# Optimization experiments

Measured on AMD Instinct MI355X. Metric: run time of the kernel, lower is better.

Reference implementation:

```python
import jax, jax.numpy as jnp
import numpy as np

N = 50000      # nodes
E = 800000     # edges
IN = 128       # in_channels
HID = 128      # hidden_channels
OUT = 2        # out_channels (edge classes)
HEADS = 8      # EGConv default num_heads
BASES = 4      # EGConv default num_bases
FH = HID // HEADS  # per-head feature dim = 16


def _egconv(x, Wb, Wc, bc, b, row, col, norm, n):
    """One EGConv layer (aggregators=['symnorm']), self-loops already in row/col/norm.
    Wb: [in, BASES*FH] basis projection (no bias).
    Wc: [in, HEADS*BASES], bc: combination weights linear.
    b : [HID] output bias.
    """
    bases = x @ Wb                                            # [n, BASES*FH]
    msg = bases[row] * norm[:, None]                          # gather + symnorm scale
    agg = jax.ops.segment_sum(msg, col, num_segments=n)       # scatter-add -> [n, BASES*FH]
    w = (x @ Wc + bc).reshape(n, HEADS, BASES)                # per-node combination weights
    out = jnp.einsum('nhb,nbf->nhf', w, agg.reshape(n, BASES, FH))
    return out.reshape(n, HEADS * FH) + b


def setup_inputs() -> dict:
    key = jax.random.key(0)
    ks = jax.random.split(key, 12)
    s = 0.05
    inp = {
        'x': jax.random.normal(ks[0], (N, IN), jnp.float32),
        'edge_index': jax.random.randint(ks[1], (2, E), 0, N, jnp.int64),
        # conv1
        'Wb1': jax.random.normal(ks[2], (IN, BASES * FH), jnp.float32) * s,
        'Wc1': jax.random.normal(ks[3], (IN, HEADS * BASES), jnp.float32) * s,
        'bc1': jnp.zeros((HEADS * BASES,), jnp.float32),
        'b1': jnp.zeros((HID,), jnp.float32),
        # conv2
        'Wb2': jax.random.normal(ks[4], (HID, BASES * FH), jnp.float32) * s,
        'Wc2': jax.random.normal(ks[5], (HID, HEADS * BASES), jnp.float32) * s,
        'bc2': jnp.zeros((HEADS * BASES,), jnp.float32),
        'b2': jnp.zeros((HID,), jnp.float32),
        # edge classifier
        'Wcls': jax.random.normal(ks[6], (2 * HID, OUT), jnp.float32) * s,
        'bcls': jnp.zeros((OUT,), jnp.float32),
    }
    return inp


def reference(x, edge_index, Wb1, Wc1, bc1, b1, Wb2, Wc2, bc2, b2, Wcls, bcls):
    n = x.shape[0]
    # add self loops (EGConv default add_self_loops=True) + gcn_norm symnorm weights
    sl = jnp.arange(n, dtype=edge_index.dtype)
    row = jnp.concatenate([edge_index[0], sl])
    col = jnp.concatenate([edge_index[1], sl])
    deg = jax.ops.segment_sum(jnp.ones(row.shape[0], x.dtype), col, num_segments=n)
    dis = jnp.where(deg > 0, deg, 1.0) ** -0.5
    dis = jnp.where(deg > 0, dis, 0.0)
    norm = dis[row] * dis[col]                                # symnorm edge weight

    h = jax.nn.relu(_egconv(x, Wb1, Wc1, bc1, b1, row, col, norm, n))
    h = _egconv(h, Wb2, Wc2, bc2, b2, row, col, norm, n)

    # edge classifier: gather endpoint embeddings of ORIGINAL edges, concat, linear
    e = jnp.concatenate([h[edge_index[0]], h[edge_index[1]]], axis=-1)  # [E, 2*HID]
    return e @ Wcls + bcls
```

## Files before the change

kernel.cpp:

```cpp
#include <hip/hip_runtime.h>
#include <hip/hip_fp16.h>

#define NN 50000
#define NNP 50048
#define EE 800000
#define CH 32
#define CHE (EE / CH)
#define NB_E2 1563
#define NWIN 4
#define WIN 12500
#define EPB 1024
#define NCHUNK 782

__global__ __launch_bounds__(256) void k_count(
    const int* __restrict__ ei, unsigned* __restrict__ pk, int* __restrict__ part)
{
    __shared__ int hist[WIN];
    int c = blockIdx.x >> 2;
    int w = blockIdx.x & 3;
    int tid = threadIdx.x;
    for (int i = tid; i < WIN; i += 256) hist[i] = 0;
    __syncthreads();
    int e0 = c * CHE;
    unsigned lo = w * WIN;
    const int* cols = ei + EE + e0;
    for (int i = tid; i < CHE / 4; i += 256) {
        int4 cc = *(const int4*)(cols + i * 4);
        unsigned d;
        d = (unsigned)cc.x - lo;
        if (d < WIN) {
            int r = atomicAdd(&hist[d], 1);
            pk[e0 + i * 4 + 0] = (unsigned)cc.x | ((unsigned)c << 16) | ((unsigned)r << 21);
        }
        d = (unsigned)cc.y - lo;
        if (d < WIN) {
            int r = atomicAdd(&hist[d], 1);
            pk[e0 + i * 4 + 1] = (unsigned)cc.y | ((unsigned)c << 16) | ((unsigned)r << 21);
        }
        d = (unsigned)cc.z - lo;
        if (d < WIN) {
            int r = atomicAdd(&hist[d], 1);
            pk[e0 + i * 4 + 2] = (unsigned)cc.z | ((unsigned)c << 16) | ((unsigned)r << 21);
        }
        d = (unsigned)cc.w - lo;
        if (d < WIN) {
            int r = atomicAdd(&hist[d], 1);
            pk[e0 + i * 4 + 3] = (unsigned)cc.w | ((unsigned)c << 16) | ((unsigned)r << 21);
        }
    }
    __syncthreads();
    int* pc = part + (size_t)c * NNP + lo;
    for (int i = tid; i < WIN; i += 256) pc[i] = hist[i];
}

__global__ void k_reduce(const int* __restrict__ part, int* __restrict__ cnt,
                         float* __restrict__ dis) {
    int i = blockIdx.x * 256 + threadIdx.x;
    if (i >= NN) return;
    int v = 0;
#pragma unroll
    for (int c = 0; c < CH; c++) v += part[(size_t)c * NNP + i];
    cnt[i] = v;
    dis[i] = rsqrtf((float)v + 1.0f);
}

__global__ void k_scan(const int* __restrict__ cnt, const int* __restrict__ part,
                       int2* __restrict__ sd, int* __restrict__ chunkstart, int n) {
    __shared__ int s[256];
    int tid = threadIdx.x, b = blockIdx.x;
    int i = b * 256 + tid;
    int v = (i < n) ? cnt[i] : 0;
    s[tid] = v;
    __syncthreads();
    for (int off = 1; off < 256; off <<= 1) {
        int t2 = (tid >= off) ? s[tid - off] : 0;
        __syncthreads();
        if (tid >= off) s[tid] += t2;
        __syncthreads();
    }
    int loc = s[tid] - v;
    int lim = b * 256;
    int pre = 0;
    for (int j = tid * 4; j < lim; j += 1024) {
        int4 c4 = *(const int4*)(cnt + j);
        pre += c4.x + c4.y + c4.z + c4.w;
    }
    __syncthreads();
    s[tid] = pre;
    __syncthreads();
    for (int off = 128; off; off >>= 1) {
        if (tid < off) s[tid] += s[tid + off];
        __syncthreads();
    }
    int boff = s[0];
    if (i < n) {
        int st = loc + boff;
        sd[i] = make_int2(st, v);
        int cs = st;
#pragma unroll
        for (int c = 0; c < CH; c++) {
            chunkstart[(size_t)c * NNP + i] = cs;
            cs += part[(size_t)c * NNP + i];
        }
    }
}

__global__ __launch_bounds__(256) void k_fill(
    const int* __restrict__ ei, const unsigned* __restrict__ pk,
    const int* __restrict__ chunkstart, int* __restrict__ csr)
{
    int w = blockIdx.x & (NWIN - 1);
    int chunk = blockIdx.x >> 2;
    int base = chunk * EPB + threadIdx.x * 4;
    unsigned lo = w * WIN;
    if (base + 3 < EE) {
        int4 rr = *(const int4*)(ei + base);
        uint4 pp = *(const uint4*)(pk + base);
        unsigned c0 = pp.x & 0xffffu, c1 = pp.y & 0xffffu;
        unsigned c2 = pp.z & 0xffffu, c3 = pp.w & 0xffffu;
        if (c0 - lo < WIN) csr[chunkstart[(size_t)((pp.x >> 16) & 31u) * NNP + c0] + (pp.x >> 21)] = rr.x;
        if (c1 - lo < WIN) csr[chunkstart[(size_t)((pp.y >> 16) & 31u) * NNP + c1] + (pp.y >> 21)] = rr.y;
        if (c2 - lo < WIN) csr[chunkstart[(size_t)((pp.z >> 16) & 31u) * NNP + c2] + (pp.z >> 21)] = rr.z;
        if (c3 - lo < WIN) csr[chunkstart[(size_t)((pp.w >> 16) & 31u) * NNP + c3] + (pp.w >> 21)] = rr.w;
    } else {
        for (int e = 0; e < 4; e++) {
            int t = base + e;
            if (t < EE) {
                unsigned pv = pk[t];
                unsigned cgl = pv & 0xffffu;
                if (cgl - lo < WIN)
                    csr[chunkstart[(size_t)((pv >> 16) & 31u) * NNP + cgl] + (pv >> 21)] = ei[t];
            }
        }
    }
}

__global__ __launch_bounds__(256) void k_gemm(
    const float* __restrict__ x, const float* __restrict__ Wb,
    const float* __restrict__ Wc, const float* __restrict__ bc,
    const float* __restrict__ dis,
    __half* __restrict__ bsh, float* __restrict__ wcomb, int n)
{
    int tid = threadIdx.x;
    int grp = blockIdx.y;
    int row = blockIdx.x * 256 + tid;
    bool valid = row < n;
    const float* xr = x + (size_t)(valid ? row : (n - 1)) * 128;

    const float* W = (grp < 2) ? (Wb + grp * 32) : Wc;
    const int ldw = (grp < 2) ? 64 : 32;

    float acc[32];
#pragma unroll
    for (int c = 0; c < 32; c++) acc[c] = 0.f;

    for (int s = 0; s < 4; s++) {
        float4 v[8];
#pragma unroll
        for (int j = 0; j < 8; j++)
            v[j] = *(const float4*)(xr + s * 32 + j * 4);
        const float* Ws = W + s * 32 * ldw;
#pragma unroll 8
        for (int k = 0; k < 32; k++) {
            float xs = ((const float*)v)[k];
            const float* wk = Ws + k * ldw;
#pragma unroll
            for (int c = 0; c < 32; c++) acc[c] = fmaf(xs, wk[c], acc[c]);
        }
    }

    if (!valid) return;
    if (grp < 2) {
        float d = dis[row];
        __half2 hh[16];
#pragma unroll
        for (int c = 0; c < 16; c++)
            hh[c] = __floats2half2_rn(acc[2 * c] * d, acc[2 * c + 1] * d);
        uint4* bo = (uint4*)(bsh + (size_t)row * 64 + grp * 32);
        const uint4* src = (const uint4*)hh;
#pragma unroll
        for (int c = 0; c < 4; c++) bo[c] = src[c];
    } else {
        float4* wo = (float4*)(wcomb + (size_t)row * 32);
#pragma unroll
        for (int c = 0; c < 8; c++)
            wo[c] = make_float4(acc[4*c] + bc[4*c], acc[4*c+1] + bc[4*c+1],
                                acc[4*c+2] + bc[4*c+2], acc[4*c+3] + bc[4*c+3]);
    }
}

template<int LAYER2>
__global__ __launch_bounds__(256) void k_agg(
    const int* __restrict__ csr, const int2* __restrict__ sd,
    const __half* __restrict__ bsh, const float* __restrict__ dis,
    const float* __restrict__ wcomb, const float* __restrict__ bias,
    float* __restrict__ h,
    const float* __restrict__ Wcls, const float* __restrict__ bcls,
    float* __restrict__ p, int n)
{
    int wid = (blockIdx.x * 256 + threadIdx.x) >> 6;
    int lane = threadIdx.x & 63;
    if (wid >= n) return;
    int2 s2 = sd[wid];
    int start = s2.x, deg = s2.y;
    int g = lane >> 4, q = lane & 15;

    const uint2* bsp = (const uint2*)bsh;
    float4 acc4 = make_float4(0.f, 0.f, 0.f, 0.f);
    if (g == 0) {
        uint2 v = bsp[(size_t)wid * 16 + q];
        float2 lo = __half22float2(*(const __half2*)&v.x);
        float2 hi = __half22float2(*(const __half2*)&v.y);
        acc4 = make_float4(lo.x, lo.y, hi.x, hi.y);
    }

    int j = 0;
    int ia = 0, ib = 0;
    if (8 <= deg) { ia = csr[start + g]; ib = csr[start + 4 + g]; }
    while (j + 8 <= deg) {
        int jn = j + 8;
        int na = 0, nb = 0;
        if (jn + 8 <= deg) { na = csr[start + jn + g]; nb = csr[start + jn + 4 + g]; }
        uint2 v0 = bsp[(size_t)ia * 16 + q];
        uint2 v1 = bsp[(size_t)ib * 16 + q];
        float2 l0 = __half22float2(*(const __half2*)&v0.x);
        float2 h0 = __half22float2(*(const __half2*)&v0.y);
        float2 l1 = __half22float2(*(const __half2*)&v1.x);
        float2 h1 = __half22float2(*(const __half2*)&v1.y);
        acc4.x += l0.x + l1.x;
        acc4.y += l0.y + l1.y;
        acc4.z += h0.x + h1.x;
        acc4.w += h0.y + h1.y;
        ia = na; ib = nb; j = jn;
    }
    int last = start + deg - 1;
    for (; j < deg; j += 4) {
        int idx = start + j + g;
        int r = csr[min(idx, last)];
        uint2 v = bsp[(size_t)r * 16 + q];
        float2 lo = __half22float2(*(const __half2*)&v.x);
        float2 hi = __half22float2(*(const __half2*)&v.y);
        float m = (j + g < deg) ? 1.f : 0.f;
        acc4.x = fmaf(lo.x, m, acc4.x);
        acc4.y = fmaf(lo.y, m, acc4.y);
        acc4.z = fmaf(hi.x, m, acc4.z);
        acc4.w = fmaf(hi.y, m, acc4.w);
    }

    acc4.x += __shfl_xor(acc4.x, 16, 64);
    acc4.y += __shfl_xor(acc4.y, 16, 64);
    acc4.z += __shfl_xor(acc4.z, 16, 64);
    acc4.w += __shfl_xor(acc4.w, 16, 64);
    acc4.x += __shfl_xor(acc4.x, 32, 64);
    acc4.y += __shfl_xor(acc4.y, 32, 64);
    acc4.z += __shfl_xor(acc4.z, 32, 64);
    acc4.w += __shfl_xor(acc4.w, 32, 64);

    float d = dis[wid];
    acc4.x *= d; acc4.y *= d; acc4.z *= d; acc4.w *= d;

    int src = lane >> 2;
    float t0 = __shfl(acc4.x, src, 64);
    float t1 = __shfl(acc4.y, src, 64);
    float t2 = __shfl(acc4.z, src, 64);
    float t3 = __shfl(acc4.w, src, 64);
    int c = lane & 3;
    float acc = (c == 0) ? t0 : (c == 1) ? t1 : (c == 2) ? t2 : t3;

    int fh = lane & 15;
    float a0 = __shfl(acc, fh, 64);
    float a1 = __shfl(acc, 16 + fh, 64);
    float a2 = __shfl(acc, 32 + fh, 64);
    float a3 = __shfl(acc, 48 + fh, 64);
    const float* wn = wcomb + (size_t)wid * 32;
    int hd = lane >> 4;
    float s1 = bias[lane];
    float s2v = bias[64 + lane];
    s1 = fmaf(wn[hd * 4 + 0], a0, s1);
    s1 = fmaf(wn[hd * 4 + 1], a1, s1);
    s1 = fmaf(wn[hd * 4 + 2], a2, s1);
    s1 = fmaf(wn[hd * 4 + 3], a3, s1);
    s2v = fmaf(wn[(4 + hd) * 4 + 0], a0, s2v);
    s2v = fmaf(wn[(4 + hd) * 4 + 1], a1, s2v);
    s2v = fmaf(wn[(4 + hd) * 4 + 2], a2, s2v);
    s2v = fmaf(wn[(4 + hd) * 4 + 3], a3, s2v);

    if (!LAYER2) {
        s1 = fmaxf(s1, 0.f);
        s2v = fmaxf(s2v, 0.f);
        h[(size_t)wid * 128 + lane] = s1;
        h[(size_t)wid * 128 + 64 + lane] = s2v;
    } else {
        float r0 = s1 * Wcls[lane * 2 + 0] + s2v * Wcls[(64 + lane) * 2 + 0];
        float r1 = s1 * Wcls[lane * 2 + 1] + s2v * Wcls[(64 + lane) * 2 + 1];
        float r2 = s1 * Wcls[(128 + lane) * 2 + 0] + s2v * Wcls[(192 + lane) * 2 + 0];
        float r3 = s1 * Wcls[(128 + lane) * 2 + 1] + s2v * Wcls[(192 + lane) * 2 + 1];
#pragma unroll
        for (int off = 32; off; off >>= 1) {
            r0 += __shfl_xor(r0, off, 64);
            r1 += __shfl_xor(r1, off, 64);
            r2 += __shfl_xor(r2, off, 64);
            r3 += __shfl_xor(r3, off, 64);
        }
        if (lane == 0) {
            p[wid * 4 + 0] = r0 + bcls[0];
            p[wid * 4 + 1] = r1 + bcls[1];
            p[wid * 4 + 2] = r2;
            p[wid * 4 + 3] = r3;
        }
    }
}

__global__ void k_edge(const int* __restrict__ ei, const float* __restrict__ p,
                       float* __restrict__ out)
{
    int t = blockIdx.x * blockDim.x + threadIdx.x;
    if (t >= EE / 2) return;
    int2 rr = *(const int2*)(ei + 2 * t);
    int2 cc = *(const int2*)(ei + EE + 2 * t);
    float2 pt0 = *(const float2*)(p + rr.x * 4);
    float2 pt1 = *(const float2*)(p + rr.y * 4);
    float2 pb0 = *(const float2*)(p + cc.x * 4 + 2);
    float2 pb1 = *(const float2*)(p + cc.y * 4 + 2);
    float4 o;
    o.x = pt0.x + pb0.x;
    o.y = pt0.y + pb0.y;
    o.z = pt1.x + pb1.x;
    o.w = pt1.y + pb1.y;
    *(float4*)(out + (size_t)t * 4) = o;
}

extern "C" void kernel_launch(void* const* d_in, const int* in_sizes, int n_in,
                              void* d_out, int out_size, void* d_ws, size_t ws_size,
                              hipStream_t stream) {
    const float* x    = (const float*)d_in[0];
    const int*   ei   = (const int*)d_in[1];
    const float* Wb1  = (const float*)d_in[2];
    const float* Wc1  = (const float*)d_in[3];
    const float* bc1  = (const float*)d_in[4];
    const float* b1   = (const float*)d_in[5];
    const float* Wb2  = (const float*)d_in[6];
    const float* Wc2  = (const float*)d_in[7];
    const float* bc2  = (const float*)d_in[8];
    const float* b2   = (const float*)d_in[9];
    const float* Wcls = (const float*)d_in[10];
    const float* bcls = (const float*)d_in[11];
    float* out = (float*)d_out;

    char* ws = (char*)d_ws;
    size_t off = 0;
    auto alloc = [&](size_t bytes) {
        void* pp = ws + off;
        off += (bytes + 15) & ~(size_t)15;
        return pp;
    };

    float*    dis    = (float*)alloc(50048 * 4);
    __half*   bsh    = (__half*)alloc((size_t)NN * 64 * 2);
    float*    wcomb  = (float*)alloc((size_t)NN * 32 * 4);
    float*    h      = (float*)alloc((size_t)NN * 128 * 4);
    float*    p      = (float*)alloc((size_t)NN * 4 * 4);
    int*      cnt    = (int*)alloc(50048 * 4);
    int2*     sd     = (int2*)alloc((size_t)50048 * 8);
    int*      csr    = (int*)alloc((size_t)EE * 4);
    unsigned* pk     = (unsigned*)alloc((size_t)EE * 4);
    int*      part   = (int*)alloc((size_t)CH * NNP * 4);
    int*      chunkstart = (int*)alloc((size_t)CH * NNP * 4);

    const int B = 256;
    int gN   = (NN + B - 1) / B;
    int gN64 = (NN * 64) / B;
    dim3 gG(gN, 3);

    k_count<<<CH * NWIN, B, 0, stream>>>(ei, pk, part);
    k_reduce<<<gN, B, 0, stream>>>(part, cnt, dis);
    k_scan<<<gN, B, 0, stream>>>(cnt, part, sd, chunkstart, NN);
    k_fill<<<NCHUNK * NWIN, B, 0, stream>>>(ei, pk, chunkstart, csr);

    k_gemm<<<gG, B, 0, stream>>>(x, Wb1, Wc1, bc1, dis, bsh, wcomb, NN);
    k_agg<0><<<gN64, B, 0, stream>>>(csr, sd, bsh, dis, wcomb, b1, h,
                                     Wcls, bcls, p, NN);

    k_gemm<<<gG, B, 0, stream>>>(h, Wb2, Wc2, bc2, dis, bsh, wcomb, NN);
    k_agg<1><<<gN64, B, 0, stream>>>(csr, sd, bsh, dis, wcomb, b2, h,
                                     Wcls, bcls, p, NN);

    k_edge<<<NB_E2, B, 0, stream>>>(ei, p, out);
}
```

Measured before the change: 292.7 us.

## Stage x tiles into LDS via async global_load_lds with double buffering

The node-feature GEMM now copies each 256-row by 32-column slice of x into shared memory with direct global-to-LDS loads, using an XOR swizzle, and prefetches the next slice into a second buffer while the current one is consumed. Previously each thread loaded its own row with strided float4 loads, so accesses within a wavefront were uncoalesced. The change adds 64KB of LDS per block, which lowers occupancy, and adds a barrier per stage. There is also a possible race: the prefetch into the other buffer is issued before the barrier that guarantees its previous contents are consumed, and the loads are not explicitly waited on before use.

```diff
diff --git a/kernel.cpp b/kernel.cpp
--- a/kernel.cpp
+++ b/kernel.cpp
@@ -135,17 +135,23 @@
     }
 }
 
+#define GLOAD_LDS16(g, l) __builtin_amdgcn_global_load_lds( \
+    (const __attribute__((address_space(1))) void*)(g),     \
+    (__attribute__((address_space(3))) void*)(l), 16, 0, 0)
+
 __global__ __launch_bounds__(256) void k_gemm(
     const float* __restrict__ x, const float* __restrict__ Wb,
     const float* __restrict__ Wc, const float* __restrict__ bc,
     const float* __restrict__ dis,
     __half* __restrict__ bsh, float* __restrict__ wcomb, int n)
 {
+    __shared__ float buf[2][256 * 32];
     int tid = threadIdx.x;
     int grp = blockIdx.y;
-    int row = blockIdx.x * 256 + tid;
+    int row0 = blockIdx.x * 256;
+    int row = row0 + tid;
     bool valid = row < n;
-    const float* xr = x + (size_t)(valid ? row : (n - 1)) * 128;
+    float d = valid ? dis[row] : 0.f;
 
     const float* W = (grp < 2) ? (Wb + grp * 32) : Wc;
     const int ldw = (grp < 2) ? 64 : 32;
@@ -154,24 +160,49 @@
 #pragma unroll
     for (int c = 0; c < 32; c++) acc[c] = 0.f;
 
+    auto issue = [&](int b, int s) {
+#pragma unroll
+        for (int i = 0; i < 8; i++) {
+            int sidx = i * 256 + tid;
+            int r = sidx >> 3;
+            int k4 = (sidx & 7) ^ (r & 7);
+            int gr = row0 + r;
+            if (gr >= n) gr = n - 1;
+            const float* src = x + (size_t)gr * 128 + s * 32 + k4 * 4;
+            float* dst = &buf[b][(size_t)(i * 256 + (tid & ~63)) * 4];
+            GLOAD_LDS16(src, dst);
+        }
+    };
+
+    issue(0, 0);
+    __syncthreads();
+
     for (int s = 0; s < 4; s++) {
-        float4 v[8];
-#pragma unroll
-        for (int j = 0; j < 8; j++)
-            v[j] = *(const float4*)(xr + s * 32 + j * 4);
+        if (s < 3) issue((s + 1) & 1, s + 1);
         const float* Ws = W + s * 32 * ldw;
-#pragma unroll 8
-        for (int k = 0; k < 32; k++) {
-            float xs = ((const float*)v)[k];
-            const float* wk = Ws + k * ldw;
-#pragma unroll
-            for (int c = 0; c < 32; c++) acc[c] = fmaf(xs, wk[c], acc[c]);
-        }
+        const float* bp = buf[s & 1];
+#pragma unroll
+        for (int j = 0; j < 8; j++) {
+            int slot = tid * 8 + (j ^ (tid & 7));
+            float4 v = *(const float4*)(bp + (size_t)slot * 4);
+            const float* wk0 = Ws + (j * 4 + 0) * ldw;
+            const float* wk1 = Ws + (j * 4 + 1) * ldw;
+            const float* wk2 = Ws + (j * 4 + 2) * ldw;
+            const float* wk3 = Ws + (j * 4 + 3) * ldw;
+#pragma unroll
+            for (int c = 0; c < 32; c++) acc[c] = fmaf(v.x, wk0[c], acc[c]);
+#pragma unroll
+            for (int c = 0; c < 32; c++) acc[c] = fmaf(v.y, wk1[c], acc[c]);
+#pragma unroll
+            for (int c = 0; c < 32; c++) acc[c] = fmaf(v.z, wk2[c], acc[c]);
+#pragma unroll
+            for (int c = 0; c < 32; c++) acc[c] = fmaf(v.w, wk3[c], acc[c]);
+        }
+        __syncthreads();
     }
 
     if (!valid) return;
     if (grp < 2) {
-        float d = dis[row];
         __half2 hh[16];
 #pragma unroll
         for (int c = 0; c < 16; c++)
```

New measurement: 329.3 us. 1.13x slower.
